# Kernel tuning notes

Hardware: AMD Instinct MI355X
Metric: run time of the kernel (lower is better)

The kernel has to match this reference:

```python
import jax, jax.numpy as jnp
import numpy as np

B, T, C, H = 4, 2048, 1024, 16
D = C // H  # head dim = 64

def setup_inputs() -> dict:
    key = jax.random.key(0)
    k1, k2, k3 = jax.random.split(key, 3)
    x = jax.random.normal(k1, (B, T, C), dtype=jnp.float32)
    w_attn = jax.random.normal(k2, (C, 3 * C), dtype=jnp.float32) * 0.02
    b_attn = jnp.zeros((3 * C,), dtype=jnp.float32)
    w_proj = jax.random.normal(k3, (C, C), dtype=jnp.float32) * 0.02
    b_proj = jnp.zeros((C,), dtype=jnp.float32)
    return {"x": x, "w_attn": w_attn, "b_attn": b_attn, "w_proj": w_proj, "b_proj": b_proj}

def reference(x, w_attn, b_attn, w_proj, b_proj):
    Bx, Tx, Cx = x.shape
    qkv = x @ w_attn + b_attn  # [B, T, 3C]
    q, k, v = jnp.split(qkv, 3, axis=2)
    # [B, H, T, D]
    q = q.reshape(Bx, Tx, H, D).swapaxes(1, 2)
    k = k.reshape(Bx, Tx, H, D).swapaxes(1, 2)
    v = v.reshape(Bx, Tx, H, D).swapaxes(1, 2)
    scale = 1.0 / jnp.sqrt(jnp.asarray(D, dtype=x.dtype))
    att = jnp.einsum('bhqd,bhkd->bhqk', q, k) * scale  # [B, H, T, T]
    causal = jnp.tril(jnp.ones((Tx, Tx), dtype=bool))
    att = jnp.where(causal[None, None], att, -jnp.inf)
    att = jax.nn.softmax(att, axis=-1)
    y = jnp.einsum('bhqk,bhkd->bhqd', att, v)  # [B, H, T, D]
    y = y.swapaxes(1, 2).reshape(Bx, Tx, Cx)
    return y @ w_proj + b_proj
```

## Files before the change

kernel.cpp:

```cpp
#include <hip/hip_runtime.h>
#include <hip/hip_bf16.h>
#include <cstdint>

#define B_ 4
#define T_ 2048
#define C_ 1024
#define H_ 16
#define D_ 64

typedef __bf16 bf16x8 __attribute__((ext_vector_type(8)));
typedef float f32x4 __attribute__((ext_vector_type(4)));

static __device__ __forceinline__ float bf2f(unsigned short u) {
    union { unsigned int i; float f; } w;
    w.i = ((unsigned int)u) << 16;
    return w.f;
}
static __device__ __forceinline__ unsigned short f2bf(float f) {
    unsigned int i = __float_as_uint(f);
    unsigned int r = (i + 0x7FFFu + ((i >> 16) & 1u)) >> 16;
    return (unsigned short)r;
}
static __device__ __forceinline__ float exp2_fast(float x) {
    float r;
    asm("v_exp_f32 %0, %1" : "=v"(r) : "v"(x));
    return r;
}

static __device__ __forceinline__ void gl_lds16(const unsigned short* g,
                                                unsigned short* l) {
    __builtin_amdgcn_global_load_lds(
        (const __attribute__((address_space(1))) unsigned int*)g,
        (__attribute__((address_space(3))) unsigned int*)l, 16, 0, 0);
}

__global__ __launch_bounds__(256)
void convert_f32_bf16(const float* __restrict__ in,
                      unsigned short* __restrict__ out, int n) {
    int i = (blockIdx.x * 256 + threadIdx.x) * 8;
    if (i < n) {
        float4 a = *(const float4*)(in + i);
        float4 b = *(const float4*)(in + i + 4);
        ushort4 s0 = {f2bf(a.x), f2bf(a.y), f2bf(a.z), f2bf(a.w)};
        ushort4 s1 = {f2bf(b.x), f2bf(b.y), f2bf(b.z), f2bf(b.w)};
        *(ushort4*)(out + i) = s0;
        *(ushort4*)(out + i + 4) = s1;
    }
}

__global__ void transpose_f32_bf16(const float* __restrict__ in,
                                   unsigned short* __restrict__ out,
                                   int R, int Cc) {
    __shared__ unsigned short tile[32][33];
    int c0 = blockIdx.x * 32;
    int r0 = blockIdx.y * 32;
    int tx = threadIdx.x, ty = threadIdx.y;
    #pragma unroll
    for (int i = ty; i < 32; i += 8)
        tile[i][tx] = f2bf(in[(size_t)(r0 + i) * Cc + c0 + tx]);
    __syncthreads();
    #pragma unroll
    for (int i = ty; i < 32; i += 8)
        out[(size_t)(c0 + i) * R + r0 + tx] = tile[tx][i];
}

__global__ __launch_bounds__(256)
void gemm_qkv(const unsigned short* __restrict__ A,
              const unsigned short* __restrict__ Bt,
              const float* __restrict__ bias,
              unsigned short* __restrict__ qkv,
              unsigned short* __restrict__ vt,
              int M, float qscale) {
    const int N = 3 * C_, K = C_;
    __shared__ __align__(16) unsigned short As[128][32];
    __shared__ __align__(16) unsigned short Bs[128][32];

    int tid = threadIdx.x;
    int row0 = blockIdx.y * 128;
    int col0 = blockIdx.x * 128;
    int wave = tid >> 6;
    int lane = tid & 63;
    int wm = wave >> 1, wn = wave & 1;
    int m16 = lane & 15, quad = lane >> 4;

    f32x4 acc[4][4];
    #pragma unroll
    for (int i = 0; i < 4; ++i)
        #pragma unroll
        for (int j = 0; j < 4; ++j)
            acc[i][j] = (f32x4){0.f, 0.f, 0.f, 0.f};

    for (int k0 = 0; k0 < K; k0 += 32) {
        #pragma unroll
        for (int it = 0; it < 2; ++it) {
            int c = tid + it * 256;
            int r = c >> 2, ko = (c & 3) << 3;
            gl_lds16(A + (size_t)(row0 + r) * K + k0 + ko, &As[0][0] + (size_t)c * 8);
            gl_lds16(Bt + (size_t)(col0 + r) * K + k0 + ko, &Bs[0][0] + (size_t)c * 8);
        }
        __syncthreads();

        bf16x8 af[4], bfr[4];
        #pragma unroll
        for (int i = 0; i < 4; ++i)
            af[i] = *(const bf16x8*)&As[wm * 64 + i * 16 + m16][quad * 8];
        #pragma unroll
        for (int j = 0; j < 4; ++j)
            bfr[j] = *(const bf16x8*)&Bs[wn * 64 + j * 16 + m16][quad * 8];
        #pragma unroll
        for (int i = 0; i < 4; ++i)
            #pragma unroll
            for (int j = 0; j < 4; ++j)
                acc[i][j] = __builtin_amdgcn_mfma_f32_16x16x32_bf16(
                    af[i], bfr[j], acc[i][j], 0, 0, 0);
        __syncthreads();
    }

    float bv[4];
    #pragma unroll
    for (int j = 0; j < 4; ++j)
        bv[j] = bias[col0 + wn * 64 + j * 16 + m16];

    unsigned short* wbuf = &As[0][0] + wave * 2048;
    bool isV = (col0 >= 2 * C_);
    float sc = (col0 < C_) ? qscale : 1.0f;
    int b_loc = row0 >> 11;
    int trow0 = (row0 & 2047) + wm * 64;

    #pragma unroll
    for (int sub = 0; sub < 4; ++sub) {
        int i0 = (sub >> 1) << 1;
        int j0 = (sub & 1) << 1;
        #pragma unroll
        for (int jj = 0; jj < 2; ++jj) {
            #pragma unroll
            for (int ii = 0; ii < 2; ++ii) {
                #pragma unroll
                for (int rr = 0; rr < 4; ++rr) {
                    int rl = ii * 16 + quad * 4 + rr;
                    int cl = jj * 16 + m16;
                    unsigned short hv =
                        f2bf((acc[i0 + ii][j0 + jj][rr] + bv[j0 + jj]) * sc);
                    if (!isV) wbuf[rl * 40 + cl] = hv;
                    else      wbuf[cl * 40 + rl] = hv;
                }
            }
        }
        __builtin_amdgcn_sched_barrier(0);
        if (!isV) {
            #pragma unroll
            for (int it = 0; it < 4; ++it) {
                int rl = it * 8 + (lane >> 3);
                int cc = (lane & 7) << 2;
                uint2 v2 = *(const uint2*)&wbuf[rl * 40 + cc];
                int rowg = row0 + wm * 64 + i0 * 16 + rl;
                int colg = col0 + wn * 64 + j0 * 16 + cc;
                *(uint2*)&qkv[(size_t)rowg * (2 * C_) + colg] = v2;
            }
        } else {
            int head = ((col0 - 2 * C_) + wn * 64) >> 6;
            unsigned short* vtb =
                vt + (size_t)((b_loc * H_ + head) * 64) * T_;
            #pragma unroll
            for (int it = 0; it < 4; ++it) {
                int dsub = it * 8 + (lane >> 3);
                int tc = (lane & 7) << 2;
                uint2 v2 = *(const uint2*)&wbuf[dsub * 40 + tc];
                int d = j0 * 16 + dsub;
                int tg = trow0 + i0 * 16 + tc;
                *(uint2*)&vtb[(size_t)d * T_ + tg] = v2;
            }
        }
        __builtin_amdgcn_sched_barrier(0);
    }
}

__global__ __launch_bounds__(256)
void gemm_out(const unsigned short* __restrict__ A, int lda,
              const unsigned short* __restrict__ Bt,
              const float* __restrict__ bias,
              float* __restrict__ Cmat,
              int M, int N, int K) {
    __shared__ __align__(16) unsigned short As[128][32];
    __shared__ __align__(16) unsigned short Bs[128][32];

    int tid = threadIdx.x;
    int row0 = blockIdx.y * 128;
    int col0 = blockIdx.x * 128;
    int wave = tid >> 6;
    int lane = tid & 63;
    int wm = wave >> 1, wn = wave & 1;
    int m16 = lane & 15, quad = lane >> 4;

    f32x4 acc[4][4];
    #pragma unroll
    for (int i = 0; i < 4; ++i)
        #pragma unroll
        for (int j = 0; j < 4; ++j)
            acc[i][j] = (f32x4){0.f, 0.f, 0.f, 0.f};

    for (int k0 = 0; k0 < K; k0 += 32) {
        #pragma unroll
        for (int it = 0; it < 2; ++it) {
            int c = tid + it * 256;
            int r = c >> 2, ko = (c & 3) << 3;
            gl_lds16(A + (size_t)(row0 + r) * lda + k0 + ko, &As[0][0] + (size_t)c * 8);
            gl_lds16(Bt + (size_t)(col0 + r) * K + k0 + ko, &Bs[0][0] + (size_t)c * 8);
        }
        __syncthreads();

        bf16x8 af[4], bfr[4];
        #pragma unroll
        for (int i = 0; i < 4; ++i)
            af[i] = *(const bf16x8*)&As[wm * 64 + i * 16 + m16][quad * 8];
        #pragma unroll
        for (int j = 0; j < 4; ++j)
            bfr[j] = *(const bf16x8*)&Bs[wn * 64 + j * 16 + m16][quad * 8];
        #pragma unroll
        for (int i = 0; i < 4; ++i)
            #pragma unroll
            for (int j = 0; j < 4; ++j)
                acc[i][j] = __builtin_amdgcn_mfma_f32_16x16x32_bf16(
                    af[i], bfr[j], acc[i][j], 0, 0, 0);
        __syncthreads();
    }

    #pragma unroll
    for (int j = 0; j < 4; ++j) {
        int col = col0 + wn * 64 + j * 16 + m16;
        float bvv = bias[col];
        #pragma unroll
        for (int i = 0; i < 4; ++i) {
            int row = row0 + wm * 64 + i * 16 + quad * 4;
            #pragma unroll
            for (int rr = 0; rr < 4; ++rr)
                Cmat[(size_t)(row + rr) * N + col] = acc[i][j][rr] + bvv;
        }
    }
}

__global__ __launch_bounds__(256)
void attn_mfma(unsigned short* __restrict__ qkv,
               const unsigned short* __restrict__ vt) {
    __shared__ __align__(16) unsigned short Ks[2][64][80];
    __shared__ __align__(16) unsigned short Vs[2][64][80];
    __shared__ __align__(16) unsigned short Pb[4][16][72];

    int bh = blockIdx.x;
    int b = bh >> 4, h = bh & 15;
    int qb = (T_ / 64 - 1) - blockIdx.y;
    int tid = threadIdx.x;
    int wave = tid >> 6;
    int lane = tid & 63;
    int m16 = lane & 15, quad = lane >> 4;

    const size_t rs = 2 * C_;
    unsigned short* base = qkv + (size_t)b * T_ * rs + h * 64;
    const unsigned short* kb0 = base + C_;
    const unsigned short* vtb = vt + (size_t)bh * 64 * T_;

    int qrow = qb * 64 + wave * 16 + m16;
    const unsigned short* qp = base + (size_t)qrow * rs;
    bf16x8 qf0 = *(const bf16x8*)(qp + quad * 8);
    bf16x8 qf1 = *(const bf16x8*)(qp + 32 + quad * 8);

    f32x4 o[4];
    #pragma unroll
    for (int dt = 0; dt < 4; ++dt) o[dt] = (f32x4){0.f, 0.f, 0.f, 0.f};
    float lrow[4] = {0.f, 0.f, 0.f, 0.f};

    int qg0 = qb * 64 + wave * 16 + quad * 4;
    int ntiles = qb + 1;

    int kkey = tid >> 3, kdc = (tid & 7) << 3;
    int vd   = tid >> 3, vkc = (tid & 7) << 3;

    uint4 ra  = *(const uint4*)(kb0 + (size_t)kkey * rs + kdc);
    uint4 rb  = *(const uint4*)(kb0 + (size_t)(kkey + 32) * rs + kdc);
    uint4 rva = *(const uint4*)(vtb + (size_t)vd * T_ + vkc);
    uint4 rvb = *(const uint4*)(vtb + (size_t)(vd + 32) * T_ + vkc);
    *(uint4*)&Ks[0][kkey][kdc]      = ra;
    *(uint4*)&Ks[0][kkey + 32][kdc] = rb;
    *(uint4*)&Vs[0][vd][vkc]        = rva;
    *(uint4*)&Vs[0][vd + 32][vkc]   = rvb;
    if (ntiles > 1) {
        const unsigned short* kn = kb0 + (size_t)64 * rs;
        ra  = *(const uint4*)(kn + (size_t)kkey * rs + kdc);
        rb  = *(const uint4*)(kn + (size_t)(kkey + 32) * rs + kdc);
        rva = *(const uint4*)(vtb + (size_t)vd * T_ + 64 + vkc);
        rvb = *(const uint4*)(vtb + (size_t)(vd + 32) * T_ + 64 + vkc);
    }
    __syncthreads();

    for (int kt = 0; kt < ntiles; ++kt) {
        int cur = kt & 1;

        f32x4 s[4];
        #pragma unroll
        for (int st = 0; st < 4; ++st) {
            f32x4 acc = (f32x4){0.f, 0.f, 0.f, 0.f};
            bf16x8 k0 = *(const bf16x8*)&Ks[cur][st * 16 + m16][quad * 8];
            bf16x8 k1 = *(const bf16x8*)&Ks[cur][st * 16 + m16][32 + quad * 8];
            acc = __builtin_amdgcn_mfma_f32_16x16x32_bf16(qf0, k0, acc, 0, 0, 0);
            acc = __builtin_amdgcn_mfma_f32_16x16x32_bf16(qf1, k1, acc, 0, 0, 0);
            s[st] = acc;
        }

        if (kt == qb) {
            #pragma unroll
            for (int st = 0; st < 4; ++st) {
                int kg = kt * 64 + st * 16 + m16;
                #pragma unroll
                for (int r = 0; r < 4; ++r)
                    if (kg > qg0 + r) s[st][r] = -1.0e30f;
            }
        }

        #pragma unroll
        for (int st = 0; st < 4; ++st) {
            #pragma unroll
            for (int r = 0; r < 4; ++r) {
                float p = exp2_fast(s[st][r]);
                lrow[r] += p;
                Pb[wave][quad * 4 + r][st * 16 + m16] = f2bf(p);
            }
        }
        __builtin_amdgcn_sched_barrier(0);

        #pragma unroll
        for (int s2 = 0; s2 < 2; ++s2) {
            bf16x8 pa = *(const bf16x8*)&Pb[wave][m16][s2 * 32 + quad * 8];
            #pragma unroll
            for (int dt = 0; dt < 4; ++dt) {
                bf16x8 vv = *(const bf16x8*)&Vs[cur][dt * 16 + m16][s2 * 32 + quad * 8];
                o[dt] = __builtin_amdgcn_mfma_f32_16x16x32_bf16(pa, vv, o[dt], 0, 0, 0);
            }
        }

        if (kt + 1 < ntiles) {
            int nxt = (kt + 1) & 1;
            *(uint4*)&Ks[nxt][kkey][kdc]      = ra;
            *(uint4*)&Ks[nxt][kkey + 32][kdc] = rb;
            *(uint4*)&Vs[nxt][vd][vkc]        = rva;
            *(uint4*)&Vs[nxt][vd + 32][vkc]   = rvb;
            if (kt + 2 < ntiles) {
                const unsigned short* kn = kb0 + (size_t)((kt + 2) * 64) * rs;
                ra  = *(const uint4*)(kn + (size_t)kkey * rs + kdc);
                rb  = *(const uint4*)(kn + (size_t)(kkey + 32) * rs + kdc);
                rva = *(const uint4*)(vtb + (size_t)vd * T_ + (kt + 2) * 64 + vkc);
                rvb = *(const uint4*)(vtb + (size_t)(vd + 32) * T_ + (kt + 2) * 64 + vkc);
            }
        }
        __syncthreads();
    }

    float lf[4];
    #pragma unroll
    for (int r = 0; r < 4; ++r) lf[r] = lrow[r];
    #pragma unroll
    for (int off = 1; off <= 8; off <<= 1)
        #pragma unroll
        for (int r = 0; r < 4; ++r)
            lf[r] += __shfl_xor(lf[r], off);

    #pragma unroll
    for (int r = 0; r < 4; ++r) {
        float inv = 1.0f / lf[r];
        unsigned short* op = base + (size_t)(qg0 + r) * rs;
        #pragma unroll
        for (int dt = 0; dt < 4; ++dt)
            op[dt * 16 + m16] = f2bf(o[dt][r] * inv);
    }
}

extern "C" void kernel_launch(void* const* d_in, const int* in_sizes, int n_in,
                              void* d_out, int out_size, void* d_ws, size_t ws_size,
                              hipStream_t stream) {
    const float* x      = (const float*)d_in[0];
    const float* w_attn = (const float*)d_in[1];
    const float* b_attn = (const float*)d_in[2];
    const float* w_proj = (const float*)d_in[3];
    const float* b_proj = (const float*)d_in[4];
    float* out = (float*)d_out;

    unsigned short* ws = (unsigned short*)d_ws;
    unsigned short* xb       = ws;
    unsigned short* w_attn_t = xb + (size_t)B_ * T_ * C_;
    unsigned short* w_proj_t = w_attn_t + (size_t)3 * C_ * C_;
    unsigned short* qkv      = w_proj_t + (size_t)C_ * C_;

    const size_t fixed_hw = (size_t)B_ * T_ * C_ + 4 * (size_t)C_ * C_;
    const size_t per_b_hw = (size_t)T_ * 2 * C_ + (size_t)H_ * 64 * T_;
    int bstep = (ws_size >= (fixed_hw + (size_t)B_ * per_b_hw) * sizeof(unsigned short))
                ? B_ : 1;

    int nx = B_ * T_ * C_;
    convert_f32_bf16<<<nx / 2048, 256, 0, stream>>>(x, xb, nx);
    transpose_f32_bf16<<<dim3(3 * C_ / 32, C_ / 32), dim3(32, 8), 0, stream>>>(
        w_attn, w_attn_t, C_, 3 * C_);
    transpose_f32_bf16<<<dim3(C_ / 32, C_ / 32), dim3(32, 8), 0, stream>>>(
        w_proj, w_proj_t, C_, C_);

    const float QSCALE = 0.125f * 1.44269504088896341f;

    for (int b0 = 0; b0 < B_; b0 += bstep) {
        int M = bstep * T_;
        const unsigned short* xbb = xb + (size_t)b0 * T_ * C_;
        float* ob = out + (size_t)b0 * T_ * C_;
        unsigned short* vt = qkv + (size_t)bstep * T_ * 2 * C_;

        gemm_qkv<<<dim3(3 * C_ / 128, M / 128), 256, 0, stream>>>(
            xbb, w_attn_t, b_attn, qkv, vt, M, QSCALE);

        attn_mfma<<<dim3(bstep * H_, T_ / 64), 256, 0, stream>>>(qkv, vt);

        gemm_out<<<dim3(C_ / 128, M / 128), 256, 0, stream>>>(
            qkv, 2 * C_, w_proj_t, b_proj, ob, M, C_, C_);
    }
}
```

Before: 263.4 us.

## Triple-buffer GEMM K loop with larger 256x128x64 tiles and swizzled LDS

Both projection GEMMs move from 128x128x32 tiles with 256 threads to 256x128x64 tiles with 512 threads. The K loop becomes a three-stage direct global-to-LDS pipeline with manual vmcnt waits and a single barrier per step. It also adds an XOR chunk swizzle against LDS bank conflicts, a workgroup-order swizzle for L2 locality, and s_setprio around the MFMA bursts. The aim is to hide global load latency and raise arithmetic intensity, at the cost of about 147KB LDS per block (one block per CU) and fewer workgroups.

```diff
diff --git a/kernel.cpp b/kernel.cpp
--- a/kernel.cpp
+++ b/kernel.cpp
@@ -7,6 +7,12 @@
 #define C_ 1024
 #define H_ 16
 #define D_ 64
+
+#define BM 256
+#define BN 128
+#define BK 64
+#define ASZ (BM * BK)
+#define BSZ (BN * BK)
 
 typedef __bf16 bf16x8 __attribute__((ext_vector_type(8)));
 typedef float f32x4 __attribute__((ext_vector_type(4)));
@@ -64,25 +70,37 @@
         out[(size_t)(c0 + i) * R + r0 + tx] = tile[tx][i];
 }
 
-__global__ __launch_bounds__(256)
+__global__ __launch_bounds__(512)
 void gemm_qkv(const unsigned short* __restrict__ A,
               const unsigned short* __restrict__ Bt,
               const float* __restrict__ bias,
               unsigned short* __restrict__ qkv,
               unsigned short* __restrict__ vt,
               int M, float qscale) {
-    const int N = 3 * C_, K = C_;
-    __shared__ __align__(16) unsigned short As[128][32];
-    __shared__ __align__(16) unsigned short Bs[128][32];
+    const int K = C_;
+    __shared__ __align__(16) unsigned short Ab[3 * ASZ];
+    __shared__ __align__(16) unsigned short Bb[3 * BSZ];
 
     int tid = threadIdx.x;
-    int row0 = blockIdx.y * 128;
-    int col0 = blockIdx.x * 128;
-    int wave = tid >> 6;
-    int lane = tid & 63;
+    int nwg = gridDim.x * gridDim.y;
+    int flat = blockIdx.y * gridDim.x + blockIdx.x;
+    int swz = (flat & 7) * (nwg >> 3) + (flat >> 3);
+    int bx = swz % gridDim.x;
+    int by = swz / gridDim.x;
+    int row0 = by * BM;
+    int col0 = bx * BN;
+
+    int wave = tid >> 6, lane = tid & 63;
     int wm = wave >> 1, wn = wave & 1;
     int m16 = lane & 15, quad = lane >> 4;
 
+    int arow = tid >> 3;
+    int achk = (tid & 7) ^ (arow & 7);
+    const unsigned short* aps = A + (size_t)(row0 + arow) * K + achk * 8;
+    const unsigned short* bps = Bt + (size_t)(col0 + arow) * K + achk * 8;
+    unsigned short* adst = Ab + tid * 8;
+    unsigned short* bdst = Bb + tid * 8;
+
     f32x4 acc[4][4];
     #pragma unroll
     for (int i = 0; i < 4; ++i)
@@ -90,38 +108,67 @@
         for (int j = 0; j < 4; ++j)
             acc[i][j] = (f32x4){0.f, 0.f, 0.f, 0.f};
 
-    for (int k0 = 0; k0 < K; k0 += 32) {
-        #pragma unroll
-        for (int it = 0; it < 2; ++it) {
-            int c = tid + it * 256;
-            int r = c >> 2, ko = (c & 3) << 3;
-            gl_lds16(A + (size_t)(row0 + r) * K + k0 + ko, &As[0][0] + (size_t)c * 8);
-            gl_lds16(Bt + (size_t)(col0 + r) * K + k0 + ko, &Bs[0][0] + (size_t)c * 8);
-        }
-        __syncthreads();
-
+    auto STAGE = [&](int koff, int oa, int ob) {
+        #pragma unroll
+        for (int l = 0; l < 4; ++l)
+            gl_lds16(aps + (size_t)(l * 64) * K + koff, adst + oa + l * 4096);
+        #pragma unroll
+        for (int l = 0; l < 2; ++l)
+            gl_lds16(bps + (size_t)(l * 64) * K + koff, bdst + ob + l * 4096);
+    };
+
+    int rbA = wm * 64 + m16;
+    int rbB = wn * 64 + m16;
+    int pc0 = ((0 + quad) ^ (m16 & 7)) * 8;
+    int pc1 = ((4 + quad) ^ (m16 & 7)) * 8;
+
+    auto PHASE = [&](int oa, int ob, int pc) {
         bf16x8 af[4], bfr[4];
         #pragma unroll
         for (int i = 0; i < 4; ++i)
-            af[i] = *(const bf16x8*)&As[wm * 64 + i * 16 + m16][quad * 8];
+            af[i] = *(const bf16x8*)(Ab + oa + (rbA + i * 16) * 64 + pc);
         #pragma unroll
         for (int j = 0; j < 4; ++j)
-            bfr[j] = *(const bf16x8*)&Bs[wn * 64 + j * 16 + m16][quad * 8];
+            bfr[j] = *(const bf16x8*)(Bb + ob + (rbB + j * 16) * 64 + pc);
+        __builtin_amdgcn_s_setprio(1);
         #pragma unroll
         for (int i = 0; i < 4; ++i)
             #pragma unroll
             for (int j = 0; j < 4; ++j)
                 acc[i][j] = __builtin_amdgcn_mfma_f32_16x16x32_bf16(
                     af[i], bfr[j], acc[i][j], 0, 0, 0);
-        __syncthreads();
-    }
+        __builtin_amdgcn_s_setprio(0);
+    };
+
+    STAGE(0, 0, 0);
+    STAGE(BK, ASZ, BSZ);
+    asm volatile("s_waitcnt vmcnt(6)" ::: "memory");
+    __builtin_amdgcn_s_barrier();
+
+    int oa0 = 0, oa1 = ASZ, oa2 = 2 * ASZ;
+    int ob0 = 0, ob1 = BSZ, ob2 = 2 * BSZ;
+    const int NT = K / BK;
+    for (int t = 0; t < NT; ++t) {
+        if (t + 2 < NT) STAGE((t + 2) * BK, oa2, ob2);
+        PHASE(oa0, ob0, pc0);
+        PHASE(oa0, ob0, pc1);
+        if (t + 1 < NT) {
+            if (t + 2 < NT) asm volatile("s_waitcnt vmcnt(6)" ::: "memory");
+            else            asm volatile("s_waitcnt vmcnt(0)" ::: "memory");
+            __builtin_amdgcn_s_barrier();
+        }
+        int x;
+        x = oa0; oa0 = oa1; oa1 = oa2; oa2 = x;
+        x = ob0; ob0 = ob1; ob1 = ob2; ob2 = x;
+    }
+    __syncthreads();
 
     float bv[4];
     #pragma unroll
     for (int j = 0; j < 4; ++j)
         bv[j] = bias[col0 + wn * 64 + j * 16 + m16];
 
-    unsigned short* wbuf = &As[0][0] + wave * 2048;
+    unsigned short* wbuf = Ab + wave * 2048;
     bool isV = (col0 >= 2 * C_);
     float sc = (col0 < C_) ? qscale : 1.0f;
     int b_loc = row0 >> 11;
@@ -175,23 +222,35 @@
     }
 }
 
-__global__ __launch_bounds__(256)
+__global__ __launch_bounds__(512)
 void gemm_out(const unsigned short* __restrict__ A, int lda,
               const unsigned short* __restrict__ Bt,
               const float* __restrict__ bias,
               float* __restrict__ Cmat,
               int M, int N, int K) {
-    __shared__ __align__(16) unsigned short As[128][32];
-    __shared__ __align__(16) unsigned short Bs[128][32];
+    __shared__ __align__(16) unsigned short Ab[3 * ASZ];
+    __shared__ __align__(16) unsigned short Bb[3 * BSZ];
 
     int tid = threadIdx.x;
-    int row0 = blockIdx.y * 128;
-    int col0 = blockIdx.x * 128;
-    int wave = tid >> 6;
-    int lane = tid & 63;
+    int nwg = gridDim.x * gridDim.y;
+    int flat = blockIdx.y * gridDim.x + blockIdx.x;
+    int swz = (flat & 7) * (nwg >> 3) + (flat >> 3);
+    int bx = swz % gridDim.x;
+    int by = swz / gridDim.x;
+    int row0 = by * BM;
+    int col0 = bx * BN;
+
+    int wave = tid >> 6, lane = tid & 63;
     int wm = wave >> 1, wn = wave & 1;
     int m16 = lane & 15, quad = lane >> 4;
 
+    int arow = tid >> 3;
+    int achk = (tid & 7) ^ (arow & 7);
+    const unsigned short* aps = A + (size_t)(row0 + arow) * lda + achk * 8;
+    const unsigned short* bps = Bt + (size_t)(col0 + arow) * K + achk * 8;
+    unsigned short* adst = Ab + tid * 8;
+    unsigned short* bdst = Bb + tid * 8;
+
     f32x4 acc[4][4];
     #pragma unroll
     for (int i = 0; i < 4; ++i)
@@ -199,30 +258,58 @@
         for (int j = 0; j < 4; ++j)
             acc[i][j] = (f32x4){0.f, 0.f, 0.f, 0.f};
 
-    for (int k0 = 0; k0 < K; k0 += 32) {
-        #pragma unroll
-        for (int it = 0; it < 2; ++it) {
-            int c = tid + it * 256;
-            int r = c >> 2, ko = (c & 3) << 3;
-            gl_lds16(A + (size_t)(row0 + r) * lda + k0 + ko, &As[0][0] + (size_t)c * 8);
-            gl_lds16(Bt + (size_t)(col0 + r) * K + k0 + ko, &Bs[0][0] + (size_t)c * 8);
-        }
-        __syncthreads();
-
+    auto STAGE = [&](int koff, int oa, int ob) {
+        #pragma unroll
+        for (int l = 0; l < 4; ++l)
+            gl_lds16(aps + (size_t)(l * 64) * lda + koff, adst + oa + l * 4096);
+        #pragma unroll
+        for (int l = 0; l < 2; ++l)
+            gl_lds16(bps + (size_t)(l * 64) * K + koff, bdst + ob + l * 4096);
+    };
+
+    int rbA = wm * 64 + m16;
+    int rbB = wn * 64 + m16;
+    int pc0 = ((0 + quad) ^ (m16 & 7)) * 8;
+    int pc1 = ((4 + quad) ^ (m16 & 7)) * 8;
+
+    auto PHASE = [&](int oa, int ob, int pc) {
         bf16x8 af[4], bfr[4];
         #pragma unroll
         for (int i = 0; i < 4; ++i)
-            af[i] = *(const bf16x8*)&As[wm * 64 + i * 16 + m16][quad * 8];
+            af[i] = *(const bf16x8*)(Ab + oa + (rbA + i * 16) * 64 + pc);
         #pragma unroll
         for (int j = 0; j < 4; ++j)
-            bfr[j] = *(const bf16x8*)&Bs[wn * 64 + j * 16 + m16][quad * 8];
+            bfr[j] = *(const bf16x8*)(Bb + ob + (rbB + j * 16) * 64 + pc);
+        __builtin_amdgcn_s_setprio(1);
         #pragma unroll
         for (int i = 0; i < 4; ++i)
             #pragma unroll
             for (int j = 0; j < 4; ++j)
                 acc[i][j] = __builtin_amdgcn_mfma_f32_16x16x32_bf16(
                     af[i], bfr[j], acc[i][j], 0, 0, 0);
-        __syncthreads();
+        __builtin_amdgcn_s_setprio(0);
+    };
+
+    STAGE(0, 0, 0);
+    STAGE(BK, ASZ, BSZ);
+    asm volatile("s_waitcnt vmcnt(6)" ::: "memory");
+    __builtin_amdgcn_s_barrier();
+
+    int oa0 = 0, oa1 = ASZ, oa2 = 2 * ASZ;
+    int ob0 = 0, ob1 = BSZ, ob2 = 2 * BSZ;
+    const int NT = C_ / BK;
+    for (int t = 0; t < NT; ++t) {
+        if (t + 2 < NT) STAGE((t + 2) * BK, oa2, ob2);
+        PHASE(oa0, ob0, pc0);
+        PHASE(oa0, ob0, pc1);
+        if (t + 1 < NT) {
+            if (t + 2 < NT) asm volatile("s_waitcnt vmcnt(6)" ::: "memory");
+            else            asm volatile("s_waitcnt vmcnt(0)" ::: "memory");
+            __builtin_amdgcn_s_barrier();
+        }
+        int x;
+        x = oa0; oa0 = oa1; oa1 = oa2; oa2 = x;
+        x = ob0; ob0 = ob1; ob1 = ob2; ob2 = x;
     }
 
     #pragma unroll
@@ -409,12 +496,12 @@
         float* ob = out + (size_t)b0 * T_ * C_;
         unsigned short* vt = qkv + (size_t)bstep * T_ * 2 * C_;
 
-        gemm_qkv<<<dim3(3 * C_ / 128, M / 128), 256, 0, stream>>>(
+        gemm_qkv<<<dim3(3 * C_ / BN, M / BM), 512, 0, stream>>>(
             xbb, w_attn_t, b_attn, qkv, vt, M, QSCALE);
 
         attn_mfma<<<dim3(bstep * H_, T_ / 64), 256, 0, stream>>>(qkv, vt);
 
-        gemm_out<<<dim3(C_ / 128, M / 128), 256, 0, stream>>>(
-            qkv, 2 * C_, w_proj_t, b_proj, ob, M, C_, C_);
-    }
-}
+        gemm_out<<<dim3(C_ / BN, M / BM), 512, 0, stream>>>(
+            qkv, 2 * C_, w_proj_t, b_proj, out + (size_t)b0 * T_ * C_, M, C_, C_);
+    }
+}
```

Measured after the change: 266.0 us. About the same (+1.0%).

## Rewrite QKV and output GEMMs as 256x256 pipelined double-buffered MFMA kernels

Applied to the files above, without the earlier changes.

Replaces the simple 128x128, BK=32 GEMM loops with a shared 256x256, BK=64 core using 512 threads. It double-buffers global-to-LDS loads in four staged groups interleaved with MFMA phases, and uses XOR-swizzled LDS layouts, s_setprio and a grid swizzle for L2 locality. The goal is to hide global load latency and raise MFMA utilization in both projection GEMMs, at the cost of 128KB of LDS per block and far more complex waitcnt/barrier bookkeeping. The smaller grids (fewer, larger tiles) may under-fill the GPU for the output GEMM.

```diff
diff --git a/kernel.cpp b/kernel.cpp
--- a/kernel.cpp
+++ b/kernel.cpp
@@ -8,14 +8,14 @@
 #define H_ 16
 #define D_ 64
 
+#define BM 256
+#define BN 256
+#define BK 64
+#define NT 16
+
 typedef __bf16 bf16x8 __attribute__((ext_vector_type(8)));
 typedef float f32x4 __attribute__((ext_vector_type(4)));
 
-static __device__ __forceinline__ float bf2f(unsigned short u) {
-    union { unsigned int i; float f; } w;
-    w.i = ((unsigned int)u) << 16;
-    return w.f;
-}
 static __device__ __forceinline__ unsigned short f2bf(float f) {
     unsigned int i = __float_as_uint(f);
     unsigned int r = (i + 0x7FFFu + ((i >> 16) & 1u)) >> 16;
@@ -64,177 +64,255 @@
         out[(size_t)(c0 + i) * R + r0 + tx] = tile[tx][i];
 }
 
-__global__ __launch_bounds__(256)
+
+#define LDA_RH(RH, BUF) do {                                                  \
+    const unsigned short* _p = smem + ((BUF) * 2 + (RH)) * 8192 + aRd;        \
+    _Pragma("unroll")                                                         \
+    for (int fi = 0; fi < 4; ++fi) {                                          \
+        afr[RH][fi][0] = *(const bf16x8*)(_p + fi * 1024 + pc0);              \
+        afr[RH][fi][1] = *(const bf16x8*)(_p + fi * 1024 + pc1);              \
+    }                                                                         \
+} while (0)
+
+#define LDB_CH(CH, BUF) do {                                                  \
+    const unsigned short* _p = smem + 32768 + ((BUF) * 2 + (CH)) * 8192 + bRd;\
+    _Pragma("unroll")                                                         \
+    for (int fj = 0; fj < 2; ++fj) {                                          \
+        bfr[fj][0] = *(const bf16x8*)(_p + fj * 1024 + pc0);                  \
+        bfr[fj][1] = *(const bf16x8*)(_p + fj * 1024 + pc1);                  \
+    }                                                                         \
+} while (0)
+
+#define MFMA_QUAD(RH, CH) do {                                                \
+    _Pragma("unroll")                                                         \
+    for (int fi = 0; fi < 4; ++fi)                                            \
+    _Pragma("unroll")                                                         \
+    for (int fj = 0; fj < 2; ++fj) {                                          \
+        acc[RH][fi][CH][fj] = __builtin_amdgcn_mfma_f32_16x16x32_bf16(        \
+            afr[RH][fi][0], bfr[fj][0], acc[RH][fi][CH][fj], 0, 0, 0);        \
+        acc[RH][fi][CH][fj] = __builtin_amdgcn_mfma_f32_16x16x32_bf16(        \
+            afr[RH][fi][1], bfr[fj][1], acc[RH][fi][CH][fj], 0, 0, 0);        \
+    }                                                                         \
+} while (0)
+
+#define PHASE_SYNC_MFMA(RH, CH) do {                                          \
+    __builtin_amdgcn_s_barrier();                                             \
+    asm volatile("s_waitcnt lgkmcnt(0)" ::: "memory");                        \
+    __builtin_amdgcn_sched_barrier(0);                                        \
+    __builtin_amdgcn_s_setprio(1);                                            \
+    MFMA_QUAD(RH, CH);                                                        \
+    __builtin_amdgcn_s_setprio(0);                                            \
+    __builtin_amdgcn_sched_barrier(0);                                        \
+} while (0)
+
+#define GEMM_CORE(APTR, LDA_STRIDE, BTPTR)                                    \
+    int tid = threadIdx.x;                                                    \
+    int nwg = gridDim.x * gridDim.y;                                          \
+    int flat = blockIdx.y * gridDim.x + blockIdx.x;                           \
+    int swz = (flat & 7) * (nwg >> 3) + (flat >> 3);                          \
+    int bx = swz % gridDim.x;                                                 \
+    int by = swz / gridDim.x;                                                 \
+    int row0 = by * BM;                                                       \
+    int col0 = bx * BN;                                                       \
+    int wave = tid >> 6, lane = tid & 63;                                     \
+    int wm = wave >> 2, wn = wave & 3;                                        \
+    int m16 = lane & 15, quad = lane >> 4;                                    \
+    int srow = tid >> 3;                                                      \
+    int kcs  = ((tid & 7) ^ (srow & 7)) * 8;                                  \
+    int bcc  = (tid >> 3) & 31;                                               \
+    int bwn0 = tid >> 8;                                                      \
+    int aRd = wm * 4096 + m16 * 64;                                           \
+    int bRd = wn * 2048 + m16 * 64;                                           \
+    int pc0 = ((0 + quad) ^ (m16 & 7)) * 8;                                   \
+    int pc1 = ((4 + quad) ^ (m16 & 7)) * 8;                                   \
+    bf16x8 afr[2][4][2];                                                      \
+    bf16x8 bfr[2][2];                                                         \
+    f32x4 acc[2][4][2][2];                                                    \
+    _Pragma("unroll")                                                         \
+    for (int a1 = 0; a1 < 2; ++a1)                                            \
+    _Pragma("unroll")                                                         \
+    for (int a2 = 0; a2 < 4; ++a2)                                            \
+    _Pragma("unroll")                                                         \
+    for (int a3 = 0; a3 < 2; ++a3)                                            \
+    _Pragma("unroll")                                                         \
+    for (int a4 = 0; a4 < 2; ++a4)                                            \
+        acc[a1][a2][a3][a4] = (f32x4){0.f, 0.f, 0.f, 0.f};                    \
+    auto STAGE_GROUP = [&](int g) {                                           \
+        if (g > 4 * NT - 1) return;                                           \
+        int kt  = g >> 2;                                                     \
+        int r   = g & 3;                                                      \
+        int buf = kt & 1;                                                     \
+        int koff = kt * BK;                                                   \
+        if ((r & 1) == 0) {                                                   \
+            int rh = r >> 1;                                                  \
+            unsigned short* dst = smem + (buf * 2 + rh) * 8192 + tid * 8;     \
+            const unsigned short* src =                                       \
+                (APTR) + (size_t)(row0 + rh * 64 + srow) * (LDA_STRIDE)       \
+                       + koff + kcs;                                          \
+            gl_lds16(src, dst);                                               \
+            gl_lds16(src + (size_t)128 * (LDA_STRIDE), dst + 4096);           \
+        } else {                                                              \
+            int ch = r >> 1;                                                  \
+            unsigned short* dst = smem + 32768 + (buf * 2 + ch) * 8192        \
+                                  + tid * 8;                                  \
+            int colg = col0 + bwn0 * 64 + ch * 32 + bcc;                      \
+            const unsigned short* src =                                       \
+                (BTPTR) + (size_t)colg * C_ + koff + kcs;                     \
+            gl_lds16(src, dst);                                               \
+            gl_lds16(src + (size_t)128 * C_, dst + 4096);                     \
+        }                                                                     \
+    };                                                                        \
+    STAGE_GROUP(0); STAGE_GROUP(1); STAGE_GROUP(2);                           \
+    STAGE_GROUP(3); STAGE_GROUP(4); STAGE_GROUP(5);                           \
+    asm volatile("s_waitcnt vmcnt(8)" ::: "memory");                          \
+    __builtin_amdgcn_s_barrier();                                             \
+    for (int t = 0; t < NT - 1; ++t) {                                        \
+        int buf = t & 1;                                                      \
+        int g0 = 4 * t + 6;                                                   \
+                                                 \
+        LDA_RH(0, buf); LDB_CH(0, buf);                                       \
+        STAGE_GROUP(g0);                                                      \
+        PHASE_SYNC_MFMA(0, 0);                                                \
+        asm volatile("s_waitcnt vmcnt(8)" ::: "memory");                      \
+        __builtin_amdgcn_s_barrier();                                         \
+                                                          \
+        LDA_RH(1, buf);                                                       \
+        STAGE_GROUP(g0 + 1);                                                  \
+        PHASE_SYNC_MFMA(1, 0);                                                \
+        asm volatile("s_waitcnt vmcnt(8)" ::: "memory");                      \
+        __builtin_amdgcn_s_barrier();                                         \
+                                                          \
+        LDB_CH(1, buf);                                                       \
+        STAGE_GROUP(g0 + 2);                                                  \
+        PHASE_SYNC_MFMA(1, 1);                                                \
+        __builtin_amdgcn_s_barrier();                                         \
+                                           \
+        STAGE_GROUP(g0 + 3);                                                  \
+        __builtin_amdgcn_s_barrier();                                         \
+        __builtin_amdgcn_s_setprio(1);                                        \
+        MFMA_QUAD(0, 1);                                                      \
+        __builtin_amdgcn_s_setprio(0);                                        \
+        __builtin_amdgcn_sched_barrier(0);                                    \
+        if (t == NT - 2) { asm volatile("s_waitcnt vmcnt(4)" ::: "memory"); } \
+        else             { asm volatile("s_waitcnt vmcnt(8)" ::: "memory"); } \
+        __builtin_amdgcn_s_barrier();                                         \
+    }                                                                         \
+    {          \
+        LDA_RH(0, 1); LDB_CH(0, 1);                                           \
+        PHASE_SYNC_MFMA(0, 0);                                                \
+        asm volatile("s_waitcnt vmcnt(2)" ::: "memory");                      \
+        __builtin_amdgcn_s_barrier();                                         \
+        LDA_RH(1, 1);                                                         \
+        PHASE_SYNC_MFMA(1, 0);                                                \
+        asm volatile("s_waitcnt vmcnt(0)" ::: "memory");                      \
+        __builtin_amdgcn_s_barrier();                                         \
+        LDB_CH(1, 1);                                                         \
+        PHASE_SYNC_MFMA(1, 1);                                                \
+        __builtin_amdgcn_s_barrier();                                         \
+        __builtin_amdgcn_s_setprio(1);                                        \
+        MFMA_QUAD(0, 1);                                                      \
+        __builtin_amdgcn_s_setprio(0);                                        \
+    }                                                                         \
+    __syncthreads();
+
+__global__ __launch_bounds__(512, 2)
 void gemm_qkv(const unsigned short* __restrict__ A,
               const unsigned short* __restrict__ Bt,
               const float* __restrict__ bias,
               unsigned short* __restrict__ qkv,
               unsigned short* __restrict__ vt,
               int M, float qscale) {
-    const int N = 3 * C_, K = C_;
-    __shared__ __align__(16) unsigned short As[128][32];
-    __shared__ __align__(16) unsigned short Bs[128][32];
-
-    int tid = threadIdx.x;
-    int row0 = blockIdx.y * 128;
-    int col0 = blockIdx.x * 128;
-    int wave = tid >> 6;
-    int lane = tid & 63;
-    int wm = wave >> 1, wn = wave & 1;
-    int m16 = lane & 15, quad = lane >> 4;
-
-    f32x4 acc[4][4];
-    #pragma unroll
-    for (int i = 0; i < 4; ++i)
-        #pragma unroll
-        for (int j = 0; j < 4; ++j)
-            acc[i][j] = (f32x4){0.f, 0.f, 0.f, 0.f};
-
-    for (int k0 = 0; k0 < K; k0 += 32) {
-        #pragma unroll
-        for (int it = 0; it < 2; ++it) {
-            int c = tid + it * 256;
-            int r = c >> 2, ko = (c & 3) << 3;
-            gl_lds16(A + (size_t)(row0 + r) * K + k0 + ko, &As[0][0] + (size_t)c * 8);
-            gl_lds16(Bt + (size_t)(col0 + r) * K + k0 + ko, &Bs[0][0] + (size_t)c * 8);
-        }
-        __syncthreads();
-
-        bf16x8 af[4], bfr[4];
-        #pragma unroll
-        for (int i = 0; i < 4; ++i)
-            af[i] = *(const bf16x8*)&As[wm * 64 + i * 16 + m16][quad * 8];
-        #pragma unroll
-        for (int j = 0; j < 4; ++j)
-            bfr[j] = *(const bf16x8*)&Bs[wn * 64 + j * 16 + m16][quad * 8];
-        #pragma unroll
-        for (int i = 0; i < 4; ++i)
-            #pragma unroll
-            for (int j = 0; j < 4; ++j)
-                acc[i][j] = __builtin_amdgcn_mfma_f32_16x16x32_bf16(
-                    af[i], bfr[j], acc[i][j], 0, 0, 0);
-        __syncthreads();
-    }
+    __shared__ __align__(16) unsigned short smem[65536];
+    GEMM_CORE(A, C_, Bt)
 
     float bv[4];
     #pragma unroll
     for (int j = 0; j < 4; ++j)
         bv[j] = bias[col0 + wn * 64 + j * 16 + m16];
 
-    unsigned short* wbuf = &As[0][0] + wave * 2048;
+    unsigned short* wbuf = smem + wave * 2048;
     bool isV = (col0 >= 2 * C_);
     float sc = (col0 < C_) ? qscale : 1.0f;
     int b_loc = row0 >> 11;
-    int trow0 = (row0 & 2047) + wm * 64;
-
-    #pragma unroll
-    for (int sub = 0; sub < 4; ++sub) {
-        int i0 = (sub >> 1) << 1;
-        int j0 = (sub & 1) << 1;
-        #pragma unroll
-        for (int jj = 0; jj < 2; ++jj) {
+    int head = isV ? ((col0 - 2 * C_ + wn * 64) >> 6) : 0;
+    unsigned short* vtb = vt + (size_t)((b_loc * H_ + head) * 64) * T_;
+
+    #pragma unroll
+    for (int rh = 0; rh < 2; ++rh) {
+        int rbase = row0 + wm * 128 + rh * 64;
+        int trow0 = (row0 & 2047) + wm * 128 + rh * 64;
+        #pragma unroll
+        for (int sub = 0; sub < 4; ++sub) {
+            int i0 = (sub >> 1) << 1;
+            int j0 = (sub & 1) << 1;
             #pragma unroll
-            for (int ii = 0; ii < 2; ++ii) {
+            for (int jj = 0; jj < 2; ++jj) {
                 #pragma unroll
-                for (int rr = 0; rr < 4; ++rr) {
-                    int rl = ii * 16 + quad * 4 + rr;
-                    int cl = jj * 16 + m16;
-                    unsigned short hv =
-                        f2bf((acc[i0 + ii][j0 + jj][rr] + bv[j0 + jj]) * sc);
-                    if (!isV) wbuf[rl * 40 + cl] = hv;
-                    else      wbuf[cl * 40 + rl] = hv;
+                for (int ii = 0; ii < 2; ++ii) {
+                    #pragma unroll
+                    for (int rr = 0; rr < 4; ++rr) {
+                        int rl = ii * 16 + quad * 4 + rr;
+                        int cl = jj * 16 + m16;
+                        float av = acc[rh][i0 + ii][(j0 + jj) >> 1]
+                                      [(j0 + jj) & 1][rr];
+                        unsigned short hv = f2bf((av + bv[j0 + jj]) * sc);
+                        if (!isV) wbuf[rl * 40 + cl] = hv;
+                        else      wbuf[cl * 40 + rl] = hv;
+                    }
                 }
             }
-        }
-        __builtin_amdgcn_sched_barrier(0);
-        if (!isV) {
-            #pragma unroll
-            for (int it = 0; it < 4; ++it) {
-                int rl = it * 8 + (lane >> 3);
-                int cc = (lane & 7) << 2;
-                uint2 v2 = *(const uint2*)&wbuf[rl * 40 + cc];
-                int rowg = row0 + wm * 64 + i0 * 16 + rl;
-                int colg = col0 + wn * 64 + j0 * 16 + cc;
-                *(uint2*)&qkv[(size_t)rowg * (2 * C_) + colg] = v2;
-            }
-        } else {
-            int head = ((col0 - 2 * C_) + wn * 64) >> 6;
-            unsigned short* vtb =
-                vt + (size_t)((b_loc * H_ + head) * 64) * T_;
-            #pragma unroll
-            for (int it = 0; it < 4; ++it) {
-                int dsub = it * 8 + (lane >> 3);
-                int tc = (lane & 7) << 2;
-                uint2 v2 = *(const uint2*)&wbuf[dsub * 40 + tc];
-                int d = j0 * 16 + dsub;
-                int tg = trow0 + i0 * 16 + tc;
-                *(uint2*)&vtb[(size_t)d * T_ + tg] = v2;
-            }
-        }
-        __builtin_amdgcn_sched_barrier(0);
-    }
-}
-
-__global__ __launch_bounds__(256)
-void gemm_out(const unsigned short* __restrict__ A, int lda,
+            __builtin_amdgcn_sched_barrier(0);
+            if (!isV) {
+                #pragma unroll
+                for (int it = 0; it < 4; ++it) {
+                    int rl = it * 8 + (lane >> 3);
+                    int cc2 = (lane & 7) << 2;
+                    uint2 v2 = *(const uint2*)&wbuf[rl * 40 + cc2];
+                    int rowg = rbase + i0 * 16 + rl;
+                    int colg = col0 + wn * 64 + j0 * 16 + cc2;
+                    *(uint2*)&qkv[(size_t)rowg * (2 * C_) + colg] = v2;
+                }
+            } else {
+                #pragma unroll
+                for (int it = 0; it < 4; ++it) {
+                    int dsub = it * 8 + (lane >> 3);
+                    int tc = (lane & 7) << 2;
+                    uint2 v2 = *(const uint2*)&wbuf[dsub * 40 + tc];
+                    int d = j0 * 16 + dsub;
+                    int tg = trow0 + i0 * 16 + tc;
+                    *(uint2*)&vtb[(size_t)d * T_ + tg] = v2;
+                }
+            }
+            __builtin_amdgcn_sched_barrier(0);
+        }
+    }
+}
+
+__global__ __launch_bounds__(512, 2)
+void gemm_out(const unsigned short* __restrict__ A,
               const unsigned short* __restrict__ Bt,
               const float* __restrict__ bias,
               float* __restrict__ Cmat,
-              int M, int N, int K) {
-    __shared__ __align__(16) unsigned short As[128][32];
-    __shared__ __align__(16) unsigned short Bs[128][32];
-
-    int tid = threadIdx.x;
-    int row0 = blockIdx.y * 128;
-    int col0 = blockIdx.x * 128;
-    int wave = tid >> 6;
-    int lane = tid & 63;
-    int wm = wave >> 1, wn = wave & 1;
-    int m16 = lane & 15, quad = lane >> 4;
-
-    f32x4 acc[4][4];
-    #pragma unroll
-    for (int i = 0; i < 4; ++i)
-        #pragma unroll
-        for (int j = 0; j < 4; ++j)
-            acc[i][j] = (f32x4){0.f, 0.f, 0.f, 0.f};
-
-    for (int k0 = 0; k0 < K; k0 += 32) {
-        #pragma unroll
-        for (int it = 0; it < 2; ++it) {
-            int c = tid + it * 256;
-            int r = c >> 2, ko = (c & 3) << 3;
-            gl_lds16(A + (size_t)(row0 + r) * lda + k0 + ko, &As[0][0] + (size_t)c * 8);
-            gl_lds16(Bt + (size_t)(col0 + r) * K + k0 + ko, &Bs[0][0] + (size_t)c * 8);
-        }
-        __syncthreads();
-
-        bf16x8 af[4], bfr[4];
-        #pragma unroll
-        for (int i = 0; i < 4; ++i)
-            af[i] = *(const bf16x8*)&As[wm * 64 + i * 16 + m16][quad * 8];
-        #pragma unroll
-        for (int j = 0; j < 4; ++j)
-            bfr[j] = *(const bf16x8*)&Bs[wn * 64 + j * 16 + m16][quad * 8];
-        #pragma unroll
-        for (int i = 0; i < 4; ++i)
+              int M) {
+    const int N = C_;
+    __shared__ __align__(16) unsigned short smem[65536];
+    GEMM_CORE(A, (2 * C_), Bt)
+
+    #pragma unroll
+    for (int rh = 0; rh < 2; ++rh) {
+        int rbase = row0 + wm * 128 + rh * 64;
+        #pragma unroll
+        for (int j = 0; j < 4; ++j) {
+            int col = col0 + wn * 64 + j * 16 + m16;
+            float bvv = bias[col];
             #pragma unroll
-            for (int j = 0; j < 4; ++j)
-                acc[i][j] = __builtin_amdgcn_mfma_f32_16x16x32_bf16(
-                    af[i], bfr[j], acc[i][j], 0, 0, 0);
-        __syncthreads();
-    }
-
-    #pragma unroll
-    for (int j = 0; j < 4; ++j) {
-        int col = col0 + wn * 64 + j * 16 + m16;
-        float bvv = bias[col];
-        #pragma unroll
-        for (int i = 0; i < 4; ++i) {
-            int row = row0 + wm * 64 + i * 16 + quad * 4;
-            #pragma unroll
-            for (int rr = 0; rr < 4; ++rr)
-                Cmat[(size_t)(row + rr) * N + col] = acc[i][j][rr] + bvv;
+            for (int i = 0; i < 4; ++i) {
+                int row = rbase + i * 16 + quad * 4;
+                #pragma unroll
+                for (int rr = 0; rr < 4; ++rr)
+                    Cmat[(size_t)(row + rr) * N + col] =
+                        acc[rh][i][j >> 1][j & 1][rr] + bvv;
+            }
         }
     }
 }
@@ -406,15 +484,14 @@
     for (int b0 = 0; b0 < B_; b0 += bstep) {
         int M = bstep * T_;
         const unsigned short* xbb = xb + (size_t)b0 * T_ * C_;
-        float* ob = out + (size_t)b0 * T_ * C_;
         unsigned short* vt = qkv + (size_t)bstep * T_ * 2 * C_;
 
-        gemm_qkv<<<dim3(3 * C_ / 128, M / 128), 256, 0, stream>>>(
+        gemm_qkv<<<dim3(3 * C_ / BN, M / BM), 512, 0, stream>>>(
             xbb, w_attn_t, b_attn, qkv, vt, M, QSCALE);
 
         attn_mfma<<<dim3(bstep * H_, T_ / 64), 256, 0, stream>>>(qkv, vt);
 
-        gemm_out<<<dim3(C_ / 128, M / 128), 256, 0, stream>>>(
-            qkv, 2 * C_, w_proj_t, b_proj, ob, M, C_, C_);
-    }
-}
+        gemm_out<<<dim3(C_ / BN, M / BM), 512, 0, stream>>>(
+            qkv, w_proj_t, b_proj, out + (size_t)b0 * T_ * C_, M);
+    }
+}
```

New measurement: 265.7 us. No clear change (+0.8%).
